# Kernel tuning notes

Measured on AMD Instinct MI355X. Metric: run time of the kernel, lower is better.

## Reference

```python
import jax, jax.numpy as jnp
import numpy as np

INPUT_SIZE = 1024
HIDDEN_SIZE = 1024
LN_EPS = 1e-5


def setup_inputs() -> dict:
    key = jax.random.key(0)
    ks = jax.random.split(key, 8)
    bs, n = 4, 2048
    # Xavier-uniform bound for square (in=out) linear layers
    bound = float(np.sqrt(6.0 / (INPUT_SIZE + HIDDEN_SIZE)))
    x = jax.random.normal(ks[0], (bs, n, INPUT_SIZE), dtype=jnp.float32)
    wq = jax.random.uniform(ks[1], (INPUT_SIZE, HIDDEN_SIZE), jnp.float32, -bound, bound)
    wk = jax.random.uniform(ks[2], (INPUT_SIZE, HIDDEN_SIZE), jnp.float32, -bound, bound)
    wv = jax.random.uniform(ks[3], (INPUT_SIZE, HIDDEN_SIZE), jnp.float32, -bound, bound)
    bq = jnp.zeros((HIDDEN_SIZE,), jnp.float32)
    bk = jnp.zeros((HIDDEN_SIZE,), jnp.float32)
    bv = jnp.zeros((HIDDEN_SIZE,), jnp.float32)
    ln_w = jnp.ones((INPUT_SIZE,), jnp.float32)
    ln_b = jnp.zeros((INPUT_SIZE,), jnp.float32)
    return {"x": x, "wq": wq, "bq": bq, "wk": wk, "bk": bk,
            "wv": wv, "bv": bv, "ln_w": ln_w, "ln_b": ln_b}


def _layernorm(x, w, b):
    mu = jnp.mean(x, axis=-1, keepdims=True)
    var = jnp.mean(jnp.square(x - mu), axis=-1, keepdims=True)
    return (x - mu) * jax.lax.rsqrt(var + LN_EPS) * w + b


def reference(x, wq, bq, wk, bk, wv, bv, ln_w, ln_b):
    # x: [b, n, d_in]
    xn = _layernorm(x, ln_w, ln_b)
    q = jnp.einsum('bnd,dh->bnh', xn, wq) + bq
    k = jnp.einsum('bnd,dh->bnh', xn, wk) + bk
    v = jnp.einsum('bnd,dh->bnh', xn, wv) + bv
    scale = 1.0 / np.sqrt(HIDDEN_SIZE)
    att = jnp.einsum('bqh,bkh->bqk', q, k) * scale  # [b, n, n]
    att = jax.nn.softmax(att, axis=-1)
    out = jnp.einsum('bqk,bkh->bqh', att, v)  # [b, n, h]
    return (att, out)
```

## Files before the change

kernel.cpp:

```cpp
#include <hip/hip_runtime.h>
#include <stdint.h>


typedef __attribute__((ext_vector_type(8))) short short8;
typedef __attribute__((ext_vector_type(4))) float floatx4;
typedef __attribute__((ext_vector_type(4))) uint16_t u16x4;

__device__ __forceinline__ uint16_t f2bf(float f) {
    union { float f; uint32_t u; } v; v.f = f;
    uint32_t r = v.u + 0x7fffu + ((v.u >> 16) & 1u);
    return (uint16_t)(r >> 16);
}

typedef const uint32_t __attribute__((address_space(1)))* gas1_t;
typedef uint32_t __attribute__((address_space(3)))* las3_t;
__device__ __forceinline__ void gload_lds16(const uint16_t* g, uint16_t* l) {
    __builtin_amdgcn_global_load_lds((gas1_t)g, (las3_t)l, 16, 0, 0);
}

__device__ __forceinline__ void s_bar()  { asm volatile("s_barrier" ::: "memory"); }
__device__ __forceinline__ void lgkm0()  { asm volatile("s_waitcnt lgkmcnt(0)" ::: "memory"); }
template<int N> __device__ __forceinline__ void vmw() {
    asm volatile("s_waitcnt vmcnt(%0)" :: "n"(N) : "memory");
}


#define READS(BASE, KS)                                                   \
    { const uint16_t* LBp = (BASE) + ABUF;                                \
      _Pragma("unroll") for (int mi = 0; mi < MIW; ++mi)                  \
          Af[mi][KS] = *(const short8*)((BASE) + aoff + mi * 1024 +       \
                                        ((KS) ? ksg1 : ksg0));            \
      _Pragma("unroll") for (int ni = 0; ni < NIW; ++ni)                  \
          Bf[ni][KS] = *(const short8*)(LBp + boff + ni * 1024 +          \
                                        ((KS) ? ksg1 : ksg0)); }

#define MFMAS(KS)                                                         \
    __builtin_amdgcn_s_setprio(1);                                        \
    _Pragma("unroll") for (int mi = 0; mi < MIW; ++mi)                    \
    _Pragma("unroll") for (int ni = 0; ni < NIW; ++ni)                    \
        acc[mi][ni] = __builtin_amdgcn_mfma_f32_16x16x32_bf16(            \
            Af[mi][KS], Bf[ni][KS], acc[mi][ni], 0, 0, 0);                \
    __builtin_amdgcn_s_setprio(0);

template<int BN, int EPI>
__device__ __forceinline__ void gemm_core(
    const uint16_t* __restrict__ A, const uint16_t* __restrict__ Bt,
    const int K, const int NT, const int m0, const int n0,
    float* __restrict__ Cf, uint16_t* __restrict__ Cb, const int ldc,
    const float* __restrict__ bq, const float* __restrict__ bk,
    const float* __restrict__ bv, const float alpha)
{
    constexpr int ABUF  = 256 * 64;
    constexpr int BP    = BN / 64;
    constexpr int BBUF  = BN * 64;
    constexpr int BUFSZ = ABUF + BBUF;
    constexpr int OPS   = 4 + BP;
    constexpr int NBUF  = (BN == 128) ? 3 : 2;
    constexpr int WAVES_N = (BN == 128) ? 2 : 4;
    constexpr int MIW  = (BN == 128) ? 4 : 8;
    constexpr int NIW  = BN / (16 * WAVES_N);
    __shared__ uint16_t sm[NBUF * BUFSZ + 4096];
    uint16_t* const trash = sm + NBUF * BUFSZ;

    const int t = threadIdx.x;

    const int srow = t >> 3;
    const int sseg = (t & 7) ^ (srow & 7);
    const uint16_t* gA = A + (size_t)(m0 + srow) * K + sseg * 8;
    const uint16_t* gB = Bt + (size_t)(n0 + srow) * K + sseg * 8;

    auto STGALL = [&](int kt, int bi) {
        const int live = kt < NT;
        const size_t ko = (size_t)(live ? kt : 0) * 64;
        uint16_t* const db = sm + bi * BUFSZ + t * 8;
        uint16_t* const tr = trash + t * 8;
#pragma unroll
        for (int p = 0; p < 4; ++p)
            gload_lds16(gA + (size_t)(p * 64) * K + ko,
                        live ? (db + p * 4096) : tr);
#pragma unroll
        for (int p = 0; p < BP; ++p)
            gload_lds16(gB + (size_t)(p * 64) * K + ko,
                        live ? (db + ABUF + p * 4096) : tr);
    };

    const int lane = t & 63;
    const int wid  = t >> 6;
    const int wm   = wid / WAVES_N;
    const int wn   = wid % WAVES_N;
    const int quad = lane >> 4;
    const int lrow = lane & 15;
    const int swz  = lrow & 7;
    const int ksg0 = (quad ^ swz) * 8;
    const int ksg1 = ((4 + quad) ^ swz) * 8;
    const int aoff = (wm * (16 * MIW) + lrow) * 64;
    const int boff = (wn * (16 * NIW) + lrow) * 64;

    floatx4 acc[MIW][NIW];
#pragma unroll
    for (int mi = 0; mi < MIW; ++mi)
#pragma unroll
        for (int ni = 0; ni < NIW; ++ni)
            acc[mi][ni] = floatx4{0.f, 0.f, 0.f, 0.f};

    short8 Af[MIW][2];
    short8 Bf[NIW][2];

    STGALL(0, 0);
    STGALL(1, 1);
    vmw<OPS>();
    s_bar();
    READS(sm, 0);

    int bcur = 0, bstage = 2;
    for (int te = 0; te < NT; ++te) {
        const uint16_t* LA;
        const uint16_t* LAn;
        if constexpr (BN == 128) {
            LA = sm + bcur * BUFSZ;
            const int bnext = (bcur == 2) ? 0 : bcur + 1;
            LAn = sm + bnext * BUFSZ;
            STGALL(te + 2, bstage);
        } else {
            LA  = sm + (te & 1) * BUFSZ;
            LAn = sm + ((te + 1) & 1) * BUFSZ;
        }

        READS(LA, 1);
        MFMAS(0);
        lgkm0();
        if constexpr (BN != 128) {
            s_bar();
            STGALL(te + 2, te & 1);
        }
        vmw<OPS>();
        s_bar();
        READS(LAn, 0);
        MFMAS(1);

        if constexpr (BN == 128) {
            bcur   = (bcur == 2) ? 0 : bcur + 1;
            bstage = (bstage == 2) ? 0 : bstage + 1;
        }
    }

    vmw<0>();

    const int rbase = m0 + wm * (16 * MIW) + quad * 4;
    const int cbase = n0 + wn * (16 * NIW) + lrow;

    if constexpr (EPI == 1) {
        float bc[NIW];
#pragma unroll
        for (int ni = 0; ni < NIW; ++ni) {
            const int col = cbase + ni * 16;
            const int z = col >> 10;
            const float* bp = (z == 0) ? bq : ((z == 1) ? bk : bv);
            bc[ni] = bp[col & 1023];
        }
#pragma unroll
        for (int mi = 0; mi < MIW; ++mi) {
#pragma unroll
            for (int ni = 0; ni < NIW; ++ni) {
                const int row = rbase + mi * 16;
                const int col = cbase + ni * 16;
                const int z = col >> 10, h = col & 1023;
#pragma unroll
                for (int r = 0; r < 4; ++r)
                    Cb[(size_t)z * 8388608 + (size_t)(row + r) * 1024 + h] =
                        f2bf(acc[mi][ni][r] + bc[ni]);
            }
        }
    } else {
#pragma unroll
        for (int mi = 0; mi < MIW; ++mi) {
#pragma unroll
            for (int ni = 0; ni < NIW; ++ni) {
                const int row = rbase + mi * 16;
                const int col = cbase + ni * 16;
#pragma unroll
                for (int r = 0; r < 4; ++r)
                    Cf[(size_t)(row + r) * ldc + col] = acc[mi][ni][r] * alpha;
            }
        }
    }
}

__global__ __launch_bounds__(512, 2) void k_qkv(
    const uint16_t* __restrict__ xn, const uint16_t* __restrict__ wt,
    const float* __restrict__ bq, const float* __restrict__ bk,
    const float* __restrict__ bv, uint16_t* __restrict__ qkv)
{
    const int flat = blockIdx.y * 16 + blockIdx.x;
    const int s = (flat & 7) * 64 + (flat >> 3);
    const int bx = s & 15, by = s >> 4;
    gemm_core<192, 1>(xn, wt, 1024, 16, by * 256, bx * 192,
                      nullptr, qkv, 0, bq, bk, bv, 0.f);
}

__global__ __launch_bounds__(512, 2) void k_scores(
    const uint16_t* __restrict__ q, const uint16_t* __restrict__ k,
    float* __restrict__ S)
{
    const int flat = (blockIdx.z * 8 + blockIdx.y) * 16 + blockIdx.x;
    const int s = (flat & 7) * 64 + (flat >> 3);
    const int x = s & 15, y = (s >> 4) & 7, z = s >> 7;
    gemm_core<128, 0>(q + (size_t)z * 2048 * 1024, k + (size_t)z * 2048 * 1024,
                      1024, 16, y * 256, x * 128,
                      S + (size_t)z * 2048 * 2048, nullptr, 2048,
                      nullptr, nullptr, nullptr, 0.03125f);
}

__global__ __launch_bounds__(512, 2) void k_out(
    const uint16_t* __restrict__ attb, const uint16_t* __restrict__ vt,
    float* __restrict__ out)
{
    const int flat = blockIdx.z * 64 + blockIdx.y * 8 + blockIdx.x;
    const int s = (flat & 7) * 32 + (flat >> 3);
    const int z = s >> 6, y = (s >> 3) & 7, x = s & 7;
    gemm_core<128, 0>(attb + (size_t)z * 2048 * 2048, vt + (size_t)z * 1024 * 2048,
                      2048, 32, y * 256, x * 128,
                      out + (size_t)z * 2048 * 1024, nullptr, 1024,
                      nullptr, nullptr, nullptr, 1.0f);
}

__global__ __launch_bounds__(256) void k_ln(
    const float* __restrict__ x, const float* __restrict__ lw,
    const float* __restrict__ lb, uint16_t* __restrict__ xn)
{
    const int row = blockIdx.x;
    const int t = threadIdx.x;
    const float* xr = x + (size_t)row * 1024;
    const float4 xv = ((const float4*)xr)[t];
    float s  = xv.x + xv.y + xv.z + xv.w;
    float s2 = xv.x * xv.x + xv.y * xv.y + xv.z * xv.z + xv.w * xv.w;
#pragma unroll
    for (int off = 32; off > 0; off >>= 1) {
        s  += __shfl_xor(s, off);
        s2 += __shfl_xor(s2, off);
    }
    __shared__ float ps[4], ps2[4];
    const int w = t >> 6, lane = t & 63;
    if (lane == 0) { ps[w] = s; ps2[w] = s2; }
    __syncthreads();
    s  = ps[0] + ps[1] + ps[2] + ps[3];
    s2 = ps2[0] + ps2[1] + ps2[2] + ps2[3];
    const float mu  = s * (1.f / 1024.f);
    const float var = s2 * (1.f / 1024.f) - mu * mu;
    const float rs  = rsqrtf(var + 1e-5f);
    const float4 wv = ((const float4*)lw)[t];
    const float4 bv = ((const float4*)lb)[t];
    u16x4 o;
    o.x = f2bf((xv.x - mu) * rs * wv.x + bv.x);
    o.y = f2bf((xv.y - mu) * rs * wv.y + bv.y);
    o.z = f2bf((xv.z - mu) * rs * wv.z + bv.z);
    o.w = f2bf((xv.w - mu) * rs * wv.w + bv.w);
    ((u16x4*)(xn + (size_t)row * 1024))[t] = o;
}

__global__ void k_wt(const float* __restrict__ wq, const float* __restrict__ wk,
                     const float* __restrict__ wv, uint16_t* __restrict__ wt)
{
    __shared__ float tile[32][33];
    const int z = blockIdx.z;
    const float* W = (z == 0) ? wq : ((z == 1) ? wk : wv);
    uint16_t* T = wt + (size_t)z * 1024 * 1024;
    const int c0 = blockIdx.x * 32, r0 = blockIdx.y * 32;
    const int tx = threadIdx.x, ty = threadIdx.y;
#pragma unroll
    for (int i = 0; i < 4; i++)
        tile[ty + 8 * i][tx] = W[(size_t)(r0 + ty + 8 * i) * 1024 + c0 + tx];
    __syncthreads();
#pragma unroll
    for (int i = 0; i < 4; i++)
        T[(size_t)(c0 + ty + 8 * i) * 1024 + r0 + tx] = f2bf(tile[tx][ty + 8 * i]);
}

__global__ __launch_bounds__(256) void k_vt(
    const uint16_t* __restrict__ v, uint16_t* __restrict__ vt)
{
    __shared__ uint16_t tile[64][68];
    const int b = blockIdx.z;
    const uint16_t* V = v + (size_t)b * 2048 * 1024;
    uint16_t* T = vt + (size_t)b * 1024 * 2048;
    const int h0 = blockIdx.x * 64, t0 = blockIdx.y * 64;
    const int t = threadIdx.x;
    const int rr = t >> 4;
    const int cc = (t & 15) * 4;
#pragma unroll
    for (int i = 0; i < 4; i++) {
        const int tok = rr + 16 * i;
        *(u16x4*)&tile[tok][cc] =
            *(const u16x4*)&V[(size_t)(t0 + tok) * 1024 + h0 + cc];
    }
    __syncthreads();
#pragma unroll
    for (int i = 0; i < 4; i++) {
        const int h = rr + 16 * i;
        u16x4 o;
        o.x = tile[cc + 0][h];
        o.y = tile[cc + 1][h];
        o.z = tile[cc + 2][h];
        o.w = tile[cc + 3][h];
        *(u16x4*)&T[(size_t)(h0 + h) * 2048 + t0 + cc] = o;
    }
}

__global__ __launch_bounds__(256) void k_softmax(
    float* __restrict__ S, uint16_t* __restrict__ attb)
{
    const size_t row = blockIdx.x;
    float* p = S + row * 2048;
    const int t = threadIdx.x;
    float4 a = ((float4*)p)[2 * t];
    float4 b = ((float4*)p)[2 * t + 1];
    float m = fmaxf(fmaxf(fmaxf(a.x, a.y), fmaxf(a.z, a.w)),
                    fmaxf(fmaxf(b.x, b.y), fmaxf(b.z, b.w)));
#pragma unroll
    for (int off = 32; off > 0; off >>= 1) m = fmaxf(m, __shfl_xor(m, off));
    __shared__ float pm[4], pl[4];
    const int w = t >> 6, lane = t & 63;
    if (lane == 0) pm[w] = m;
    __syncthreads();
    m = fmaxf(fmaxf(pm[0], pm[1]), fmaxf(pm[2], pm[3]));

    a.x = __expf(a.x - m); a.y = __expf(a.y - m);
    a.z = __expf(a.z - m); a.w = __expf(a.w - m);
    b.x = __expf(b.x - m); b.y = __expf(b.y - m);
    b.z = __expf(b.z - m); b.w = __expf(b.w - m);
    float s = a.x + a.y + a.z + a.w + b.x + b.y + b.z + b.w;
#pragma unroll
    for (int off = 32; off > 0; off >>= 1) s += __shfl_xor(s, off);
    if (lane == 0) pl[w] = s;
    __syncthreads();
    s = pl[0] + pl[1] + pl[2] + pl[3];
    const float inv = 1.f / s;

    a.x *= inv; a.y *= inv; a.z *= inv; a.w *= inv;
    b.x *= inv; b.y *= inv; b.z *= inv; b.w *= inv;
    ((float4*)p)[2 * t]     = a;
    ((float4*)p)[2 * t + 1] = b;

    uint16_t* q = attb + row * 2048 + t * 8;
    u16x4 o0, o1;
    o0.x = f2bf(a.x); o0.y = f2bf(a.y); o0.z = f2bf(a.z); o0.w = f2bf(a.w);
    o1.x = f2bf(b.x); o1.y = f2bf(b.y); o1.z = f2bf(b.z); o1.w = f2bf(b.w);
    ((u16x4*)q)[0] = o0;
    ((u16x4*)q)[1] = o1;
}

extern "C" void kernel_launch(void* const* d_in, const int* in_sizes, int n_in,
                              void* d_out, int out_size, void* d_ws, size_t ws_size,
                              hipStream_t stream)
{
    const float* x  = (const float*)d_in[0];
    const float* wq = (const float*)d_in[1];
    const float* bq = (const float*)d_in[2];
    const float* wk = (const float*)d_in[3];
    const float* bk = (const float*)d_in[4];
    const float* wv = (const float*)d_in[5];
    const float* bv = (const float*)d_in[6];
    const float* lw = (const float*)d_in[7];
    const float* lb = (const float*)d_in[8];

    float* att = (float*)d_out;
    float* out = (float*)d_out + (size_t)16777216;

    uint16_t* xn = (uint16_t*)d_out;
    uint16_t* wt = (uint16_t*)d_out + (size_t)8388608;

    uint16_t* ws   = (uint16_t*)d_ws;
    uint16_t* q    = ws;
    uint16_t* k    = ws + (size_t)8388608;
    uint16_t* v    = ws + (size_t)2 * 8388608;
    uint16_t* vt   = ws;
    uint16_t* attb = ws + (size_t)8388608;
    uint16_t* qkv  = q;

    if (ws_size < (size_t)50331648) return;

    k_ln<<<8192, 256, 0, stream>>>(x, lw, lb, xn);
    k_wt<<<dim3(32, 32, 3), dim3(32, 8), 0, stream>>>(wq, wk, wv, wt);
    k_qkv<<<dim3(16, 32), 512, 0, stream>>>(xn, wt, bq, bk, bv, qkv);
    k_scores<<<dim3(16, 8, 4), 512, 0, stream>>>(q, k, att);
    k_vt<<<dim3(16, 32, 4), 256, 0, stream>>>(v, vt);
    k_softmax<<<8192, 256, 0, stream>>>(att, attb);
    k_out<<<dim3(8, 8, 4), 512, 0, stream>>>(attb, vt, out);
}
```

Measured before the change: 306.7 us.

## Use fat 4-wave GEMM workgroups with larger per-wave tiles and double buffering

```diff
diff --git a/kernel.cpp b/kernel.cpp
--- a/kernel.cpp
+++ b/kernel.cpp
@@ -27,7 +27,7 @@
 
 #define READS(BASE, KS)                                                   \
     { const uint16_t* LBp = (BASE) + ABUF;                                \
-      _Pragma("unroll") for (int mi = 0; mi < MIW; ++mi)                  \
+      _Pragma("unroll") for (int mi = 0; mi < 8; ++mi)                    \
           Af[mi][KS] = *(const short8*)((BASE) + aoff + mi * 1024 +       \
                                         ((KS) ? ksg1 : ksg0));            \
       _Pragma("unroll") for (int ni = 0; ni < NIW; ++ni)                  \
@@ -36,31 +36,28 @@
 
 #define MFMAS(KS)                                                         \
     __builtin_amdgcn_s_setprio(1);                                        \
-    _Pragma("unroll") for (int mi = 0; mi < MIW; ++mi)                    \
+    _Pragma("unroll") for (int mi = 0; mi < 8; ++mi)                      \
     _Pragma("unroll") for (int ni = 0; ni < NIW; ++ni)                    \
         acc[mi][ni] = __builtin_amdgcn_mfma_f32_16x16x32_bf16(            \
             Af[mi][KS], Bf[ni][KS], acc[mi][ni], 0, 0, 0);                \
     __builtin_amdgcn_s_setprio(0);
 
 template<int BN, int EPI>
-__device__ __forceinline__ void gemm_core(
+__device__ __forceinline__ void gemm_fat(
     const uint16_t* __restrict__ A, const uint16_t* __restrict__ Bt,
     const int K, const int NT, const int m0, const int n0,
     float* __restrict__ Cf, uint16_t* __restrict__ Cb, const int ldc,
     const float* __restrict__ bq, const float* __restrict__ bk,
     const float* __restrict__ bv, const float alpha)
 {
-    constexpr int ABUF  = 256 * 64;
-    constexpr int BP    = BN / 64;
+    constexpr int ABUF  = 16384;
+    constexpr int BP    = BN / 32;
     constexpr int BBUF  = BN * 64;
     constexpr int BUFSZ = ABUF + BBUF;
-    constexpr int OPS   = 4 + BP;
-    constexpr int NBUF  = (BN == 128) ? 3 : 2;
-    constexpr int WAVES_N = (BN == 128) ? 2 : 4;
-    constexpr int MIW  = (BN == 128) ? 4 : 8;
-    constexpr int NIW  = BN / (16 * WAVES_N);
-    __shared__ uint16_t sm[NBUF * BUFSZ + 4096];
-    uint16_t* const trash = sm + NBUF * BUFSZ;
+    constexpr int OPS   = 8 + BP;
+    constexpr int NIW   = BN / 32;
+    __shared__ uint16_t sm[2 * BUFSZ + 2048];
+    uint16_t* const trash = sm + 2 * BUFSZ;
 
     const int t = threadIdx.x;
 
@@ -69,41 +66,41 @@
     const uint16_t* gA = A + (size_t)(m0 + srow) * K + sseg * 8;
     const uint16_t* gB = Bt + (size_t)(n0 + srow) * K + sseg * 8;
 
-    auto STGALL = [&](int kt, int bi) {
-        const int live = kt < NT;
-        const size_t ko = (size_t)(live ? kt : 0) * 64;
-        uint16_t* const db = sm + bi * BUFSZ + t * 8;
+    auto STGALL = [&](int kt, int b) {
+        const bool lv = kt < NT;
+        const size_t ko = (size_t)(lv ? kt : 0) * 64;
+        uint16_t* const db = sm + b * BUFSZ + t * 8;
         uint16_t* const tr = trash + t * 8;
 #pragma unroll
-        for (int p = 0; p < 4; ++p)
-            gload_lds16(gA + (size_t)(p * 64) * K + ko,
-                        live ? (db + p * 4096) : tr);
+        for (int p = 0; p < 8; ++p)
+            gload_lds16(gA + (size_t)(p * 32) * K + ko,
+                        lv ? (db + p * 2048) : tr);
 #pragma unroll
         for (int p = 0; p < BP; ++p)
-            gload_lds16(gB + (size_t)(p * 64) * K + ko,
-                        live ? (db + ABUF + p * 4096) : tr);
+            gload_lds16(gB + (size_t)(p * 32) * K + ko,
+                        lv ? (db + ABUF + p * 2048) : tr);
     };
 
     const int lane = t & 63;
     const int wid  = t >> 6;
-    const int wm   = wid / WAVES_N;
-    const int wn   = wid % WAVES_N;
+    const int wm   = wid >> 1;
+    const int wn   = wid & 1;
     const int quad = lane >> 4;
     const int lrow = lane & 15;
     const int swz  = lrow & 7;
     const int ksg0 = (quad ^ swz) * 8;
     const int ksg1 = ((4 + quad) ^ swz) * 8;
-    const int aoff = (wm * (16 * MIW) + lrow) * 64;
+    const int aoff = (wm * 128 + lrow) * 64;
     const int boff = (wn * (16 * NIW) + lrow) * 64;
 
-    floatx4 acc[MIW][NIW];
-#pragma unroll
-    for (int mi = 0; mi < MIW; ++mi)
+    floatx4 acc[8][NIW];
+#pragma unroll
+    for (int mi = 0; mi < 8; ++mi)
 #pragma unroll
         for (int ni = 0; ni < NIW; ++ni)
             acc[mi][ni] = floatx4{0.f, 0.f, 0.f, 0.f};
 
-    short8 Af[MIW][2];
+    short8 Af[8][2];
     short8 Bf[NIW][2];
 
     STGALL(0, 0);
@@ -112,41 +109,24 @@
     s_bar();
     READS(sm, 0);
 
-    int bcur = 0, bstage = 2;
     for (int te = 0; te < NT; ++te) {
-        const uint16_t* LA;
-        const uint16_t* LAn;
-        if constexpr (BN == 128) {
-            LA = sm + bcur * BUFSZ;
-            const int bnext = (bcur == 2) ? 0 : bcur + 1;
-            LAn = sm + bnext * BUFSZ;
-            STGALL(te + 2, bstage);
-        } else {
-            LA  = sm + (te & 1) * BUFSZ;
-            LAn = sm + ((te + 1) & 1) * BUFSZ;
-        }
+        const uint16_t* LA  = sm + (te & 1) * BUFSZ;
+        const uint16_t* LAn = sm + ((te + 1) & 1) * BUFSZ;
 
         READS(LA, 1);
         MFMAS(0);
         lgkm0();
-        if constexpr (BN != 128) {
-            s_bar();
-            STGALL(te + 2, te & 1);
-        }
+        s_bar();
+        STGALL(te + 2, te & 1);
         vmw<OPS>();
         s_bar();
         READS(LAn, 0);
         MFMAS(1);
-
-        if constexpr (BN == 128) {
-            bcur   = (bcur == 2) ? 0 : bcur + 1;
-            bstage = (bstage == 2) ? 0 : bstage + 1;
-        }
     }
 
     vmw<0>();
 
-    const int rbase = m0 + wm * (16 * MIW) + quad * 4;
+    const int rbase = m0 + wm * 128 + quad * 4;
     const int cbase = n0 + wn * (16 * NIW) + lrow;
 
     if constexpr (EPI == 1) {
@@ -159,7 +139,7 @@
             bc[ni] = bp[col & 1023];
         }
 #pragma unroll
-        for (int mi = 0; mi < MIW; ++mi) {
+        for (int mi = 0; mi < 8; ++mi) {
 #pragma unroll
             for (int ni = 0; ni < NIW; ++ni) {
                 const int row = rbase + mi * 16;
@@ -173,7 +153,7 @@
         }
     } else {
 #pragma unroll
-        for (int mi = 0; mi < MIW; ++mi) {
+        for (int mi = 0; mi < 8; ++mi) {
 #pragma unroll
             for (int ni = 0; ni < NIW; ++ni) {
                 const int row = rbase + mi * 16;
@@ -186,7 +166,7 @@
     }
 }
 
-__global__ __launch_bounds__(512, 2) void k_qkv(
+__global__ __launch_bounds__(256, 1) void k_qkv(
     const uint16_t* __restrict__ xn, const uint16_t* __restrict__ wt,
     const float* __restrict__ bq, const float* __restrict__ bk,
     const float* __restrict__ bv, uint16_t* __restrict__ qkv)
@@ -194,34 +174,34 @@
     const int flat = blockIdx.y * 16 + blockIdx.x;
     const int s = (flat & 7) * 64 + (flat >> 3);
     const int bx = s & 15, by = s >> 4;
-    gemm_core<192, 1>(xn, wt, 1024, 16, by * 256, bx * 192,
-                      nullptr, qkv, 0, bq, bk, bv, 0.f);
-}
-
-__global__ __launch_bounds__(512, 2) void k_scores(
+    gemm_fat<192, 1>(xn, wt, 1024, 16, by * 256, bx * 192,
+                     nullptr, qkv, 0, bq, bk, bv, 0.f);
+}
+
+__global__ __launch_bounds__(256, 1) void k_scores(
     const uint16_t* __restrict__ q, const uint16_t* __restrict__ k,
     float* __restrict__ S)
 {
     const int flat = (blockIdx.z * 8 + blockIdx.y) * 16 + blockIdx.x;
     const int s = (flat & 7) * 64 + (flat >> 3);
     const int x = s & 15, y = (s >> 4) & 7, z = s >> 7;
-    gemm_core<128, 0>(q + (size_t)z * 2048 * 1024, k + (size_t)z * 2048 * 1024,
-                      1024, 16, y * 256, x * 128,
-                      S + (size_t)z * 2048 * 2048, nullptr, 2048,
-                      nullptr, nullptr, nullptr, 0.03125f);
-}
-
-__global__ __launch_bounds__(512, 2) void k_out(
+    gemm_fat<128, 0>(q + (size_t)z * 2048 * 1024, k + (size_t)z * 2048 * 1024,
+                     1024, 16, y * 256, x * 128,
+                     S + (size_t)z * 2048 * 2048, nullptr, 2048,
+                     nullptr, nullptr, nullptr, 0.03125f);
+}
+
+__global__ __launch_bounds__(256, 1) void k_out(
     const uint16_t* __restrict__ attb, const uint16_t* __restrict__ vt,
     float* __restrict__ out)
 {
     const int flat = blockIdx.z * 64 + blockIdx.y * 8 + blockIdx.x;
     const int s = (flat & 7) * 32 + (flat >> 3);
     const int z = s >> 6, y = (s >> 3) & 7, x = s & 7;
-    gemm_core<128, 0>(attb + (size_t)z * 2048 * 2048, vt + (size_t)z * 1024 * 2048,
-                      2048, 32, y * 256, x * 128,
-                      out + (size_t)z * 2048 * 1024, nullptr, 1024,
-                      nullptr, nullptr, nullptr, 1.0f);
+    gemm_fat<128, 0>(attb + (size_t)z * 2048 * 2048, vt + (size_t)z * 1024 * 2048,
+                     2048, 32, y * 256, x * 128,
+                     out + (size_t)z * 2048 * 1024, nullptr, 1024,
+                     nullptr, nullptr, nullptr, 1.0f);
 }
 
 __global__ __launch_bounds__(256) void k_ln(
@@ -381,9 +361,9 @@
 
     k_ln<<<8192, 256, 0, stream>>>(x, lw, lb, xn);
     k_wt<<<dim3(32, 32, 3), dim3(32, 8), 0, stream>>>(wq, wk, wv, wt);
-    k_qkv<<<dim3(16, 32), 512, 0, stream>>>(xn, wt, bq, bk, bv, qkv);
-    k_scores<<<dim3(16, 8, 4), 512, 0, stream>>>(q, k, att);
+    k_qkv<<<dim3(16, 32), 256, 0, stream>>>(xn, wt, bq, bk, bv, qkv);
+    k_scores<<<dim3(16, 8, 4), 256, 0, stream>>>(q, k, att);
     k_vt<<<dim3(16, 32, 4), 256, 0, stream>>>(v, vt);
     k_softmax<<<8192, 256, 0, stream>>>(att, attb);
-    k_out<<<dim3(8, 8, 4), 512, 0, stream>>>(attb, vt, out);
-}
+    k_out<<<dim3(8, 8, 4), 256, 0, stream>>>(attb, vt, out);
+}
```

New measurement: 335.7 us. 9.5% more time.

## Fuse V transpose into QKV epilogue and merge layernorm with weight transpose

Applied to the files above, without the earlier changes.

```diff
diff --git a/kernel.cpp b/kernel.cpp
--- a/kernel.cpp
+++ b/kernel.cpp
@@ -48,7 +48,8 @@
     const int K, const int NT, const int m0, const int n0,
     float* __restrict__ Cf, uint16_t* __restrict__ Cb, const int ldc,
     const float* __restrict__ bq, const float* __restrict__ bk,
-    const float* __restrict__ bv, const float alpha)
+    const float* __restrict__ bv, const float alpha,
+    uint16_t* __restrict__ vtp)
 {
     constexpr int ABUF  = 256 * 64;
     constexpr int BP    = BN / 64;
@@ -158,26 +159,51 @@
             const float* bp = (z == 0) ? bq : ((z == 1) ? bk : bv);
             bc[ni] = bp[col & 1023];
         }
+        uint16_t* const stash = sm;
+#pragma unroll
+        for (int mi = 0; mi < MIW; ++mi) {
+#pragma unroll
+            for (int ni = 0; ni < NIW; ++ni) {
+                const int col = cbase + ni * 16;
+                const int z = col >> 10;
+                if (z == 2) {
+                    const int lr = wm * (16 * MIW) + quad * 4 + mi * 16;
+#pragma unroll
+                    for (int r = 0; r < 4; ++r)
+                        stash[(col - n0) * 260 + lr + r] =
+                            f2bf(acc[mi][ni][r] + bc[ni]);
+                } else {
+                    const int row = rbase + mi * 16;
+                    const int h = col & 1023;
+#pragma unroll
+                    for (int r = 0; r < 4; ++r)
+                        Cb[(size_t)z * 8388608 + (size_t)(row + r) * 1024 + h] =
+                            f2bf(acc[mi][ni][r] + bc[ni]);
+                }
+            }
+        }
+        if (n0 + BN > 2048) {
+            lgkm0();
+            s_bar();
+            const int b  = m0 >> 11;
+            const int t0 = m0 & 2047;
+            for (int cl = wid; cl < BN; cl += 8) {
+                const int col = n0 + cl;
+                if (col >= 2048) {
+                    const u16x4 vv =
+                        *(const u16x4*)&stash[cl * 260 + lane * 4];
+                    *(u16x4*)&vtp[(size_t)b * 2097152 +
+                                  (size_t)(col - 2048) * 2048 + t0 + lane * 4] = vv;
+                }
+            }
+        }
+    } else {
 #pragma unroll
         for (int mi = 0; mi < MIW; ++mi) {
 #pragma unroll
             for (int ni = 0; ni < NIW; ++ni) {
                 const int row = rbase + mi * 16;
                 const int col = cbase + ni * 16;
-                const int z = col >> 10, h = col & 1023;
-#pragma unroll
-                for (int r = 0; r < 4; ++r)
-                    Cb[(size_t)z * 8388608 + (size_t)(row + r) * 1024 + h] =
-                        f2bf(acc[mi][ni][r] + bc[ni]);
-            }
-        }
-    } else {
-#pragma unroll
-        for (int mi = 0; mi < MIW; ++mi) {
-#pragma unroll
-            for (int ni = 0; ni < NIW; ++ni) {
-                const int row = rbase + mi * 16;
-                const int col = cbase + ni * 16;
 #pragma unroll
                 for (int r = 0; r < 4; ++r)
                     Cf[(size_t)(row + r) * ldc + col] = acc[mi][ni][r] * alpha;
@@ -189,13 +215,14 @@
 __global__ __launch_bounds__(512, 2) void k_qkv(
     const uint16_t* __restrict__ xn, const uint16_t* __restrict__ wt,
     const float* __restrict__ bq, const float* __restrict__ bk,
-    const float* __restrict__ bv, uint16_t* __restrict__ qkv)
+    const float* __restrict__ bv, uint16_t* __restrict__ qk,
+    uint16_t* __restrict__ vt)
 {
     const int flat = blockIdx.y * 16 + blockIdx.x;
     const int s = (flat & 7) * 64 + (flat >> 3);
     const int bx = s & 15, by = s >> 4;
     gemm_core<192, 1>(xn, wt, 1024, 16, by * 256, bx * 192,
-                      nullptr, qkv, 0, bq, bk, bv, 0.f);
+                      nullptr, qk, 0, bq, bk, bv, 0.f, vt);
 }
 
 __global__ __launch_bounds__(512, 2) void k_scores(
@@ -208,7 +235,7 @@
     gemm_core<128, 0>(q + (size_t)z * 2048 * 1024, k + (size_t)z * 2048 * 1024,
                       1024, 16, y * 256, x * 128,
                       S + (size_t)z * 2048 * 2048, nullptr, 2048,
-                      nullptr, nullptr, nullptr, 0.03125f);
+                      nullptr, nullptr, nullptr, 0.03125f, nullptr);
 }
 
 __global__ __launch_bounds__(512, 2) void k_out(
@@ -221,88 +248,60 @@
     gemm_core<128, 0>(attb + (size_t)z * 2048 * 2048, vt + (size_t)z * 1024 * 2048,
                       2048, 32, y * 256, x * 128,
                       out + (size_t)z * 2048 * 1024, nullptr, 1024,
-                      nullptr, nullptr, nullptr, 1.0f);
-}
-
-__global__ __launch_bounds__(256) void k_ln(
+                      nullptr, nullptr, nullptr, 1.0f, nullptr);
+}
+
+__global__ __launch_bounds__(256) void k_prep(
     const float* __restrict__ x, const float* __restrict__ lw,
-    const float* __restrict__ lb, uint16_t* __restrict__ xn)
-{
-    const int row = blockIdx.x;
+    const float* __restrict__ lb, uint16_t* __restrict__ xn,
+    const float* __restrict__ wq, const float* __restrict__ wk,
+    const float* __restrict__ wv, uint16_t* __restrict__ wt)
+{
     const int t = threadIdx.x;
-    const float* xr = x + (size_t)row * 1024;
-    const float4 xv = ((const float4*)xr)[t];
-    float s  = xv.x + xv.y + xv.z + xv.w;
-    float s2 = xv.x * xv.x + xv.y * xv.y + xv.z * xv.z + xv.w * xv.w;
-#pragma unroll
-    for (int off = 32; off > 0; off >>= 1) {
-        s  += __shfl_xor(s, off);
-        s2 += __shfl_xor(s2, off);
-    }
-    __shared__ float ps[4], ps2[4];
-    const int w = t >> 6, lane = t & 63;
-    if (lane == 0) { ps[w] = s; ps2[w] = s2; }
-    __syncthreads();
-    s  = ps[0] + ps[1] + ps[2] + ps[3];
-    s2 = ps2[0] + ps2[1] + ps2[2] + ps2[3];
-    const float mu  = s * (1.f / 1024.f);
-    const float var = s2 * (1.f / 1024.f) - mu * mu;
-    const float rs  = rsqrtf(var + 1e-5f);
-    const float4 wv = ((const float4*)lw)[t];
-    const float4 bv = ((const float4*)lb)[t];
-    u16x4 o;
-    o.x = f2bf((xv.x - mu) * rs * wv.x + bv.x);
-    o.y = f2bf((xv.y - mu) * rs * wv.y + bv.y);
-    o.z = f2bf((xv.z - mu) * rs * wv.z + bv.z);
-    o.w = f2bf((xv.w - mu) * rs * wv.w + bv.w);
-    ((u16x4*)(xn + (size_t)row * 1024))[t] = o;
-}
-
-__global__ void k_wt(const float* __restrict__ wq, const float* __restrict__ wk,
-                     const float* __restrict__ wv, uint16_t* __restrict__ wt)
-{
-    __shared__ float tile[32][33];
-    const int z = blockIdx.z;
-    const float* W = (z == 0) ? wq : ((z == 1) ? wk : wv);
-    uint16_t* T = wt + (size_t)z * 1024 * 1024;
-    const int c0 = blockIdx.x * 32, r0 = blockIdx.y * 32;
-    const int tx = threadIdx.x, ty = threadIdx.y;
-#pragma unroll
-    for (int i = 0; i < 4; i++)
-        tile[ty + 8 * i][tx] = W[(size_t)(r0 + ty + 8 * i) * 1024 + c0 + tx];
-    __syncthreads();
-#pragma unroll
-    for (int i = 0; i < 4; i++)
-        T[(size_t)(c0 + ty + 8 * i) * 1024 + r0 + tx] = f2bf(tile[tx][ty + 8 * i]);
-}
-
-__global__ __launch_bounds__(256) void k_vt(
-    const uint16_t* __restrict__ v, uint16_t* __restrict__ vt)
-{
-    __shared__ uint16_t tile[64][68];
-    const int b = blockIdx.z;
-    const uint16_t* V = v + (size_t)b * 2048 * 1024;
-    uint16_t* T = vt + (size_t)b * 1024 * 2048;
-    const int h0 = blockIdx.x * 64, t0 = blockIdx.y * 64;
-    const int t = threadIdx.x;
-    const int rr = t >> 4;
-    const int cc = (t & 15) * 4;
-#pragma unroll
-    for (int i = 0; i < 4; i++) {
-        const int tok = rr + 16 * i;
-        *(u16x4*)&tile[tok][cc] =
-            *(const u16x4*)&V[(size_t)(t0 + tok) * 1024 + h0 + cc];
-    }
-    __syncthreads();
-#pragma unroll
-    for (int i = 0; i < 4; i++) {
-        const int h = rr + 16 * i;
+    if (blockIdx.x < 8192) {
+        const int row = blockIdx.x;
+        const float* xr = x + (size_t)row * 1024;
+        const float4 xv = ((const float4*)xr)[t];
+        float s  = xv.x + xv.y + xv.z + xv.w;
+        float s2 = xv.x * xv.x + xv.y * xv.y + xv.z * xv.z + xv.w * xv.w;
+#pragma unroll
+        for (int off = 32; off > 0; off >>= 1) {
+            s  += __shfl_xor(s, off);
+            s2 += __shfl_xor(s2, off);
+        }
+        __shared__ float ps[4], ps2[4];
+        const int w = t >> 6, lane = t & 63;
+        if (lane == 0) { ps[w] = s; ps2[w] = s2; }
+        __syncthreads();
+        s  = ps[0] + ps[1] + ps[2] + ps[3];
+        s2 = ps2[0] + ps2[1] + ps2[2] + ps2[3];
+        const float mu  = s * (1.f / 1024.f);
+        const float var = s2 * (1.f / 1024.f) - mu * mu;
+        const float rs  = rsqrtf(var + 1e-5f);
+        const float4 wv4 = ((const float4*)lw)[t];
+        const float4 bv4 = ((const float4*)lb)[t];
         u16x4 o;
-        o.x = tile[cc + 0][h];
-        o.y = tile[cc + 1][h];
-        o.z = tile[cc + 2][h];
-        o.w = tile[cc + 3][h];
-        *(u16x4*)&T[(size_t)(h0 + h) * 2048 + t0 + cc] = o;
+        o.x = f2bf((xv.x - mu) * rs * wv4.x + bv4.x);
+        o.y = f2bf((xv.y - mu) * rs * wv4.y + bv4.y);
+        o.z = f2bf((xv.z - mu) * rs * wv4.z + bv4.z);
+        o.w = f2bf((xv.w - mu) * rs * wv4.w + bv4.w);
+        ((u16x4*)(xn + (size_t)row * 1024))[t] = o;
+    } else {
+        __shared__ float tile[32][33];
+        const int bid = blockIdx.x - 8192;
+        const int z = bid >> 10;
+        const int rem = bid & 1023;
+        const int c0 = (rem & 31) * 32, r0 = (rem >> 5) * 32;
+        const float* W = (z == 0) ? wq : ((z == 1) ? wk : wv);
+        uint16_t* T = wt + (size_t)z * 1024 * 1024;
+        const int tx = t & 31, ty = t >> 5;
+#pragma unroll
+        for (int i = 0; i < 4; i++)
+            tile[ty + 8 * i][tx] = W[(size_t)(r0 + ty + 8 * i) * 1024 + c0 + tx];
+        __syncthreads();
+#pragma unroll
+        for (int i = 0; i < 4; i++)
+            T[(size_t)(c0 + ty + 8 * i) * 1024 + r0 + tx] = f2bf(tile[tx][ty + 8 * i]);
     }
 }
 
@@ -372,18 +371,14 @@
     uint16_t* ws   = (uint16_t*)d_ws;
     uint16_t* q    = ws;
     uint16_t* k    = ws + (size_t)8388608;
-    uint16_t* v    = ws + (size_t)2 * 8388608;
-    uint16_t* vt   = ws;
-    uint16_t* attb = ws + (size_t)8388608;
-    uint16_t* qkv  = q;
+    uint16_t* vt   = ws + (size_t)2 * 8388608;
+    uint16_t* attb = ws;
 
     if (ws_size < (size_t)50331648) return;
 
-    k_ln<<<8192, 256, 0, stream>>>(x, lw, lb, xn);
-    k_wt<<<dim3(32, 32, 3), dim3(32, 8), 0, stream>>>(wq, wk, wv, wt);
-    k_qkv<<<dim3(16, 32), 512, 0, stream>>>(xn, wt, bq, bk, bv, qkv);
+    k_prep<<<8192 + 3072, 256, 0, stream>>>(x, lw, lb, xn, wq, wk, wv, wt);
+    k_qkv<<<dim3(16, 32), 512, 0, stream>>>(xn, wt, bq, bk, bv, q, vt);
     k_scores<<<dim3(16, 8, 4), 512, 0, stream>>>(q, k, att);
-    k_vt<<<dim3(16, 32, 4), 256, 0, stream>>>(v, vt);
     k_softmax<<<8192, 256, 0, stream>>>(att, attb);
     k_out<<<dim3(8, 8, 4), 512, 0, stream>>>(attb, vt, out);
 }
```

After: 316.6 us. 1.03x slower.
